# Kernel optimization log

Measured on AMD Instinct MI355X. Metric: run time of the kernel, lower is better.

The kernel has to match this reference:

```python
import jax, jax.numpy as jnp
import numpy as np

EPS = 1e-5
GROUPS = 32


def group_norm(x, gamma, beta):
    b, c, h, w = x.shape
    xg = x.reshape(b, GROUPS, c // GROUPS, h, w)
    mu = xg.mean(axis=(2, 3, 4), keepdims=True)
    var = xg.var(axis=(2, 3, 4), keepdims=True)
    xn = ((xg - mu) * jax.lax.rsqrt(var + EPS)).reshape(b, c, h, w)
    return xn * gamma[None, :, None, None] + beta[None, :, None, None]


def setup_inputs() -> dict:
    key = jax.random.key(0)
    ks = jax.random.split(key, 4)
    b, c, h, w = 4, 512, 64, 64
    x = jax.random.normal(ks[0], (b, c, h, w), dtype=jnp.float32)
    gn_w = jnp.ones((c,), jnp.float32)
    gn_b = jnp.zeros((c,), jnp.float32)
    qkv_w = jax.random.normal(ks[1], (3 * c, c), dtype=jnp.float32) * (c ** -0.5)
    qkv_b = jnp.zeros((3 * c,), jnp.float32)
    out_w = jax.random.normal(ks[2], (c, c), dtype=jnp.float32) * (c ** -0.5)
    out_b = jnp.zeros((c,), jnp.float32)
    return {"x": x, "gn_w": gn_w, "gn_b": gn_b, "qkv_w": qkv_w,
            "qkv_b": qkv_b, "out_w": out_w, "out_b": out_b}


def reference(x, gn_w, gn_b, qkv_w, qkv_b, out_w, out_b):
    b, c, hh, ww = x.shape
    n = hh * ww
    h = group_norm(x, gn_w, gn_b)
    # 1x1 conv == per-pixel matmul over channels
    qkv = jnp.einsum('bchw,oc->bohw', h, qkv_w) + qkv_b[None, :, None, None]
    q, k, v = jnp.split(qkv, 3, axis=1)
    q = q.transpose(0, 2, 3, 1).reshape(b, n, c)   # (b, n, c)
    k = k.reshape(b, c, n)                          # (b, c, n)
    v = v.transpose(0, 2, 3, 1).reshape(b, n, c)   # (b, n, c)
    attn = jax.nn.softmax(jnp.einsum('bnc,bcm->bnm', q, k) * (c ** -0.5), axis=-1)
    out = jnp.einsum('bnm,bmc->bnc', attn, v)
    out = out.reshape(b, hh, ww, c).transpose(0, 3, 1, 2)
    out = jnp.einsum('bchw,oc->bohw', out, out_w) + out_b[None, :, None, None]
    return out + x
```

## Files before the change

### kernel.cpp

```cpp
#include <hip/hip_runtime.h>
#include <cmath>

#define NB 4
#define NC 512
#define NN 4096
#define ATTN_SCALE 0.04419417382415922f

typedef __bf16 bf16x8 __attribute__((ext_vector_type(8)));
typedef float floatx4 __attribute__((ext_vector_type(4)));

__device__ __forceinline__ unsigned short f2bf(float f) {
    union { float f; unsigned int u; } v; v.f = f;
    return (unsigned short)((v.u + 0x7fffu + ((v.u >> 16) & 1u)) >> 16);
}
__device__ __forceinline__ unsigned short f2bf_trunc(float f) {
    union { float f; unsigned int u; } v; v.f = f;
    return (unsigned short)(v.u >> 16);
}

__device__ __forceinline__ void gload_lds16(const unsigned short* gp, unsigned short* lp) {
    __builtin_amdgcn_global_load_lds(
        (const __attribute__((address_space(1))) void*)gp,
        (__attribute__((address_space(3))) void*)lp, 16, 0, 0);
}

template<int N> __device__ __forceinline__ void wait_vmcnt() {
    if constexpr (N == 0) asm volatile("s_waitcnt vmcnt(0)" ::: "memory");
    else if constexpr (N == 2) asm volatile("s_waitcnt vmcnt(2)" ::: "memory");
    else if constexpr (N == 3) asm volatile("s_waitcnt vmcnt(3)" ::: "memory");
    else if constexpr (N == 4) asm volatile("s_waitcnt vmcnt(4)" ::: "memory");
    else if constexpr (N == 6) asm volatile("s_waitcnt vmcnt(6)" ::: "memory");
}

__global__ __launch_bounds__(256) void gn_partial_kernel(
    const float* __restrict__ x, float* __restrict__ part)
{
    int blk = blockIdx.x;
    int bg = blk >> 3, sub = blk & 7;
    const float4* xv = (const float4*)(x + (size_t)bg * 16 * NN + (size_t)sub * 8192);
    float s1 = 0.f, s2 = 0.f;
#pragma unroll
    for (int i = 0; i < 8; ++i) {
        float4 v = xv[threadIdx.x + i * 256];
        s1 += v.x + v.y + v.z + v.w;
        s2 += v.x * v.x + v.y * v.y + v.z * v.z + v.w * v.w;
    }
#pragma unroll
    for (int off = 32; off; off >>= 1) {
        s1 += __shfl_xor(s1, off, 64);
        s2 += __shfl_xor(s2, off, 64);
    }
    __shared__ float r1[4], r2[4];
    int lane = threadIdx.x & 63, w = threadIdx.x >> 6;
    if (lane == 0) { r1[w] = s1; r2[w] = s2; }
    __syncthreads();
    if (threadIdx.x == 0) {
        part[blk * 2]     = r1[0] + r1[1] + r1[2] + r1[3];
        part[blk * 2 + 1] = r2[0] + r2[1] + r2[2] + r2[3];
    }
}

__global__ __launch_bounds__(128) void gn_final_kernel(
    const float* __restrict__ part, const float* __restrict__ gw,
    const float* __restrict__ gb, float* __restrict__ ss)
{
    int tg = threadIdx.x;
    int b = tg >> 5, g = tg & 31;
    float s1 = 0.f, s2 = 0.f;
#pragma unroll
    for (int s = 0; s < 8; ++s) {
        s1 += part[(tg * 8 + s) * 2];
        s2 += part[(tg * 8 + s) * 2 + 1];
    }
    float mean = s1 * (1.0f / 65536.0f);
    float var  = s2 * (1.0f / 65536.0f) - mean * mean;
    float rstd = rsqrtf(var + 1e-5f);
#pragma unroll
    for (int i = 0; i < 16; ++i) {
        int c = g * 16 + i;
        float sc = rstd * gw[c];
        ss[b * NC + c] = sc;
        ss[2048 + b * NC + c] = gb[c] - mean * sc;
    }
}

__global__ __launch_bounds__(256) void wconv_kernel(
    const float* __restrict__ qkv_w, const float* __restrict__ out_w,
    unsigned short* __restrict__ wq, unsigned short* __restrict__ wo)
{
    int i = blockIdx.x * 256 + threadIdx.x;
    const int NQ = 1536 * 512;
    if (i < NQ) wq[i] = f2bf(qkv_w[i]);
    else        wo[i - NQ] = f2bf(out_w[i - NQ]);
}

__global__ __launch_bounds__(256) void htnorm_kernel(
    const float* __restrict__ x, const float* __restrict__ ss,
    unsigned short* __restrict__ ht)
{
    int b = blockIdx.z;
    int c0 = blockIdx.y * 32, n0 = blockIdx.x * 32;
    __shared__ float T[32][33];
    int tx = threadIdx.x & 31, ty = threadIdx.x >> 5;
    const float* xb = x + ((size_t)b * NC + c0) * NN;
    const float* sc = ss + b * NC + c0;
    const float* sh = ss + 2048 + b * NC + c0;
#pragma unroll
    for (int i = 0; i < 4; ++i) {
        int c = ty + i * 8;
        T[c][tx] = xb[(size_t)c * NN + n0 + tx] * sc[c] + sh[c];
    }
    __syncthreads();
    unsigned short* hb = ht + ((size_t)b * NN + n0) * NC + c0;
#pragma unroll
    for (int i = 0; i < 4; ++i) {
        int n = ty + i * 8;
        hb[(size_t)n * NC + tx] = f2bf(T[tx][n]);
    }
}

template<int MODE, int BM, int BN, int KD, int MINB, int PIPE>
__global__ __launch_bounds__(256, MINB) void mfma_gemm(
    const unsigned short* __restrict__ Abase,
    const unsigned short* __restrict__ Bbase,
    const float* __restrict__ e0, const float* __restrict__ e1,
    float* __restrict__ outf,
    unsigned short* __restrict__ ob0, unsigned short* __restrict__ ob1)
{
    constexpr int NT = KD / 32;
    constexpr int FI = BM / 32;
    constexpr int FJ = BN / 32;
    constexpr int LPS = BM / 64 + BN / 64;
    const size_t bnc = (size_t)NN * NC;
    const size_t bss = (size_t)NN * NN;

    int z, m0, n0;
    if constexpr (MODE == 2) {
        const int id = blockIdx.x;
        const int xcd = id & 7, j = id >> 3;
        const int mi = xcd * 8 + (j & 7);
        z = mi >> 4; m0 = (mi & 15) * BM; n0 = (j >> 3) * BN;
    } else {
        z = blockIdx.z; m0 = blockIdx.y * BM; n0 = blockIdx.x * BN;
    }

    const unsigned short* A;
    const unsigned short* B;
    if constexpr (MODE == 0)      { A = Abase + (size_t)z * bnc; B = Bbase; }
    else if constexpr (MODE == 1) { A = Abase; B = Bbase + (size_t)z * bnc; }
    else if constexpr (MODE == 2) { A = Abase + (size_t)z * bnc; B = Bbase + (size_t)z * bnc; }
    else                          { A = Abase; B = Bbase + (size_t)z * bnc; }

    __shared__ __attribute__((aligned(16))) unsigned short As[3][BM * 32];
    __shared__ __attribute__((aligned(16))) unsigned short Bs[3][BN * 32];

    const int t = threadIdx.x;
    const int lane = t & 63;
    const int w = t >> 6;
    const int wr = w >> 1, wc = w & 1;

    const int sr = w * 16 + (lane >> 2);
    const int scs = ((lane & 3) ^ ((lane >> 3) & 3)) * 8;
    const int lds_elem = w * 512;
    const int kslot = lane >> 4;

    floatx4 acc[FI][FJ] = {};

    auto stage = [&](int buf, int tile) {
        const int k0 = tile * 32;
#pragma unroll
        for (int s = 0; s < BM / 64; ++s)
            gload_lds16(A + (size_t)(m0 + s * 64 + sr) * KD + k0 + scs,
                        &As[buf][s * 2048 + lds_elem]);
#pragma unroll
        for (int s = 0; s < BN / 64; ++s)
            gload_lds16(B + (size_t)(n0 + s * 64 + sr) * KD + k0 + scs,
                        &Bs[buf][s * 2048 + lds_elem]);
    };

    auto ds_frags = [&](int buf, bf16x8* af, bf16x8* bfr) {
#pragma unroll
        for (int i = 0; i < FI; ++i) {
            const int ra = wr * (BM / 2) + i * 16 + (lane & 15);
            af[i] = *(const bf16x8*)(&As[buf][ra * 32 + ((kslot ^ ((ra >> 1) & 3)) * 8)]);
        }
#pragma unroll
        for (int j = 0; j < FJ; ++j) {
            const int rb = wc * (BN / 2) + j * 16 + (lane & 15);
            bfr[j] = *(const bf16x8*)(&Bs[buf][rb * 32 + ((kslot ^ ((rb >> 1) & 3)) * 8)]);
        }
    };

    auto mfma_all = [&](const bf16x8* af, const bf16x8* bfr) {
#pragma unroll
        for (int i = 0; i < FI; ++i)
#pragma unroll
            for (int j = 0; j < FJ; ++j)
                acc[i][j] = __builtin_amdgcn_mfma_f32_16x16x32_bf16(
                    af[i], bfr[j], acc[i][j], 0, 0, 0);
    };

    if constexpr (PIPE == 0) {
        bf16x8 af[FI], bfr[FJ];
        stage(0, 0);
        stage(1, 1);
        wait_vmcnt<LPS>();
        __builtin_amdgcn_s_barrier();
#pragma unroll
        for (int kt = 0; kt < NT - 2; ++kt) {
            stage((kt + 2) % 3, kt + 2);
            ds_frags(kt % 3, af, bfr);
            mfma_all(af, bfr);
            asm volatile("s_waitcnt lgkmcnt(0)" ::: "memory");
            wait_vmcnt<LPS>();
            __builtin_amdgcn_s_barrier();
        }
        ds_frags((NT - 2) % 3, af, bfr);
        mfma_all(af, bfr);
        asm volatile("s_waitcnt lgkmcnt(0)" ::: "memory");
        wait_vmcnt<0>();
        __builtin_amdgcn_s_barrier();
        ds_frags((NT - 1) % 3, af, bfr);
        mfma_all(af, bfr);
    } else {
        bf16x8 afA[FI], bfA[FJ], afB[FI], bfB[FJ];
        stage(0, 0);
        stage(1, 1);
        wait_vmcnt<LPS>();
        __builtin_amdgcn_s_barrier();
        ds_frags(0, afA, bfA);
        asm volatile("s_waitcnt lgkmcnt(0)" ::: "memory");
#pragma unroll
        for (int kp = 0; kp < (NT - 2) / 2; ++kp) {
            const int kt = kp * 2;
            stage((kt + 2) % 3, kt + 2);
            wait_vmcnt<LPS>();
            __builtin_amdgcn_s_barrier();
            ds_frags((kt + 1) % 3, afB, bfB);
            mfma_all(afA, bfA);
            asm volatile("s_waitcnt lgkmcnt(0)" ::: "memory");
            stage((kt + 3) % 3, kt + 3);
            wait_vmcnt<LPS>();
            __builtin_amdgcn_s_barrier();
            ds_frags((kt + 2) % 3, afA, bfA);
            mfma_all(afB, bfB);
            asm volatile("s_waitcnt lgkmcnt(0)" ::: "memory");
        }
        wait_vmcnt<0>();
        __builtin_amdgcn_s_barrier();
        ds_frags((NT - 1) % 3, afB, bfB);
        mfma_all(afA, bfA);
        asm volatile("s_waitcnt lgkmcnt(0)" ::: "memory");
        mfma_all(afB, bfB);
    }

    const int fr = lane >> 4;
    const int fc = lane & 15;

    if constexpr (MODE == 2) {
        float rs[FI][4];
#pragma unroll
        for (int i = 0; i < FI; ++i)
#pragma unroll
            for (int r = 0; r < 4; ++r) rs[i][r] = 0.f;
#pragma unroll
        for (int i = 0; i < FI; ++i) {
#pragma unroll
            for (int j = 0; j < FJ; ++j) {
                int n = n0 + wc * (BN / 2) + j * 16 + fc;
                int mbase = m0 + wr * (BM / 2) + i * 16 + fr * 4;
#pragma unroll
                for (int r = 0; r < 4; ++r) {
                    float e = __expf(acc[i][j][r]);
                    ob0[(size_t)z * bss + (size_t)(mbase + r) * NN + n] = f2bf_trunc(e);
                    rs[i][r] += e;
                }
            }
        }
#pragma unroll
        for (int i = 0; i < FI; ++i) {
#pragma unroll
            for (int r = 0; r < 4; ++r) {
                float v = rs[i][r];
                v += __shfl_xor(v, 1, 16);
                v += __shfl_xor(v, 2, 16);
                v += __shfl_xor(v, 4, 16);
                v += __shfl_xor(v, 8, 16);
                if (fc == 0) {
                    int m = m0 + wr * (BM / 2) + i * 16 + fr * 4 + r;
                    atomicAdd(&outf[z * NN + m], v);
                }
            }
        }
        return;
    }

#pragma unroll
    for (int i = 0; i < FI; ++i) {
#pragma unroll
        for (int j = 0; j < FJ; ++j) {
            int n = n0 + wc * (BN / 2) + j * 16 + fc;
            int mbase = m0 + wr * (BM / 2) + i * 16 + fr * 4;
#pragma unroll
            for (int r = 0; r < 4; ++r) {
                int m = mbase + r;
                float val = acc[i][j][r];
                if constexpr (MODE == 0) {
                    val += e0[n];
                    if (n < 512) ob0[((size_t)z * NN + m) * NC + n] = f2bf(val * ATTN_SCALE);
                    else         ob1[((size_t)z * NN + m) * NC + (n - 512)] = f2bf(val);
                } else if constexpr (MODE == 1) {
                    val += e0[1024 + m];
                    ob0[((size_t)z * NC + m) * NN + n] = f2bf(val);
                } else {
                    size_t idx = ((size_t)z * NC + m) * NN + n;
                    outf[idx] = val + e0[m] + e1[idx];
                }
            }
        }
    }
}

__global__ __launch_bounds__(256, 2) void pv_gemm(
    const unsigned short* __restrict__ Abase,
    const unsigned short* __restrict__ Bbase,
    const float* __restrict__ L,
    unsigned short* __restrict__ Ob)
{
    const int id = blockIdx.x;
    const int xcd = id & 7;
    const int j0 = id >> 3;
    const int ct = j0 & 3;
    const int p = (j0 >> 2) * 8 + xcd;
    const int ptile = p & 31, z = p >> 5;

    const size_t bss = (size_t)NN * NN, bnc = (size_t)NN * NC;
    const unsigned short* A = Abase + (size_t)z * bss;
    const unsigned short* B = Bbase + (size_t)z * bnc;
    const int m0 = ptile * 128;
    const int n0 = ct * 128;

    __shared__ __attribute__((aligned(16))) unsigned short As[2][128 * 64];
    __shared__ __attribute__((aligned(16))) unsigned short Bs[2][128 * 64];

    const int t = threadIdx.x;
    const int lane = t & 63;
    const int w = t >> 6;
    const int wr = w >> 1, wc = w & 1;

    const int sr = w * 8 + (lane >> 3);
    const int scs = ((lane & 7) ^ (lane >> 3)) * 8;
    const int lds_elem = w * 512;

    floatx4 acc[4][4] = {};

    auto stage = [&](int buf, int k0) {
#pragma unroll
        for (int s = 0; s < 4; ++s)
            gload_lds16(A + (size_t)(m0 + s * 32 + sr) * NN + k0 + scs,
                        &As[buf][s * 2048 + lds_elem]);
#pragma unroll
        for (int s = 0; s < 4; ++s)
            gload_lds16(B + (size_t)(n0 + s * 32 + sr) * NN + k0 + scs,
                        &Bs[buf][s * 2048 + lds_elem]);
    };

    auto compute = [&](int buf) {
#pragma unroll
        for (int kk = 0; kk < 2; ++kk) {
            bf16x8 af[4], bfr[4];
#pragma unroll
            for (int i = 0; i < 4; ++i) {
                const int ra = wr * 64 + i * 16 + (lane & 15);
                af[i] = *(const bf16x8*)(&As[buf][ra * 64 +
                        (((kk * 4 + (lane >> 4)) ^ (ra & 7)) * 8)]);
            }
#pragma unroll
            for (int jf = 0; jf < 4; ++jf) {
                const int rb = wc * 64 + jf * 16 + (lane & 15);
                bfr[jf] = *(const bf16x8*)(&Bs[buf][rb * 64 +
                        (((kk * 4 + (lane >> 4)) ^ (rb & 7)) * 8)]);
            }
#pragma unroll
            for (int i = 0; i < 4; ++i)
#pragma unroll
                for (int jf = 0; jf < 4; ++jf)
                    acc[i][jf] = __builtin_amdgcn_mfma_f32_16x16x32_bf16(
                        af[i], bfr[jf], acc[i][jf], 0, 0, 0);
        }
    };

    stage(0, 0);
    asm volatile("s_waitcnt vmcnt(0)" ::: "memory");
    __builtin_amdgcn_s_barrier();
    for (int kc = 0; kc < 63; ++kc) {
        stage((kc + 1) & 1, (kc + 1) * 64);
        compute(kc & 1);
        asm volatile("s_waitcnt lgkmcnt(0)" ::: "memory");
        asm volatile("s_waitcnt vmcnt(0)" ::: "memory");
        __builtin_amdgcn_s_barrier();
    }
    compute(1);

    const int fr = lane >> 4;
    const int fc = lane & 15;
#pragma unroll
    for (int i = 0; i < 4; ++i) {
#pragma unroll
        for (int r = 0; r < 4; ++r) {
            int m = m0 + wr * 64 + i * 16 + fr * 4 + r;
            float linv = 1.0f / L[z * NN + m];
#pragma unroll
            for (int jf = 0; jf < 4; ++jf) {
                int n = n0 + wc * 64 + jf * 16 + fc;
                Ob[(size_t)z * bnc + (size_t)m * NC + n] = f2bf(acc[i][jf][r] * linv);
            }
        }
    }
}

extern "C" void kernel_launch(void* const* d_in, const int* in_sizes, int n_in,
                              void* d_out, int out_size, void* d_ws, size_t ws_size,
                              hipStream_t stream)
{
    const float* x     = (const float*)d_in[0];
    const float* gn_w  = (const float*)d_in[1];
    const float* gn_b  = (const float*)d_in[2];
    const float* qkv_w = (const float*)d_in[3];
    const float* qkv_b = (const float*)d_in[4];
    const float* out_w = (const float*)d_in[5];
    const float* out_b = (const float*)d_in[6];
    float* out = (float*)d_out;

    const size_t bnc = (size_t)NN * NC;
    char* w = (char*)d_ws;
    float* ss   = (float*)w;                 w += 16384;
    float* part = (float*)w;                 w += 8192;
    float* Lsum = (float*)w;                 w += (size_t)NB * NN * 4;
    unsigned short* wq = (unsigned short*)w; w += (size_t)1536 * 512 * 2;
    unsigned short* wo = (unsigned short*)w; w += (size_t)512 * 512 * 2;
    unsigned short* qt = (unsigned short*)w; w += NB * bnc * 2;
    unsigned short* kt = (unsigned short*)w; w += NB * bnc * 2;
    unsigned short* vt = (unsigned short*)w; w += NB * bnc * 2;
    unsigned short* SP = (unsigned short*)w; w += (size_t)NB * NN * NN * 2;
    unsigned short* ht = SP;
    unsigned short* Ob = qt;

    hipMemsetAsync(Lsum, 0, (size_t)NB * NN * sizeof(float), stream);

    gn_partial_kernel<<<1024, 256, 0, stream>>>(x, part);
    gn_final_kernel<<<1, 128, 0, stream>>>(part, gn_w, gn_b, ss);
    wconv_kernel<<<(1536 * 512 + 512 * 512) / 256, 256, 0, stream>>>(qkv_w, out_w, wq, wo);
    htnorm_kernel<<<dim3(NN / 32, NC / 32, NB), 256, 0, stream>>>(x, ss, ht);

    mfma_gemm<0, 128, 128, 512, 2, 1><<<dim3(1024 / 128, NN / 128, NB), 256, 0, stream>>>(
        ht, wq, qkv_b, nullptr, nullptr, qt, kt);
    mfma_gemm<1, 64, 128, 512, 4, 1><<<dim3(NN / 128, 512 / 64, NB), 256, 0, stream>>>(
        wq + (size_t)1024 * 512, ht, qkv_b, nullptr, nullptr, vt, nullptr);

    mfma_gemm<2, 256, 128, 512, 2, 0><<<dim3(2048), 256, 0, stream>>>(
        qt, kt, nullptr, nullptr, Lsum, SP, nullptr);
    pv_gemm<<<dim3(512), 256, 0, stream>>>(SP, vt, Lsum, Ob);

    mfma_gemm<4, 64, 128, 512, 4, 1><<<dim3(NN / 128, 512 / 64, NB), 256, 0, stream>>>(
        wo, Ob, out_b, x, out, nullptr, nullptr);
}
```

Baseline: 341.6 us.

## Enlarge PV GEMM tile to 256x128 with 512 threads and triple-buffered loads

The P·V GEMM kernel now uses 512-thread blocks, each computing a 256x128 output tile. The launch grid halves to 256 blocks, and the block-to-tile mapping changes so each XCD pair handles a single batch. The single-stage double buffer becomes a three-deep ring with partial vmcnt waits, so two chunks are in flight while one is computed. The aim is better reuse of the B tile, a lower count of redundant A/B loads, and hidden global-load latency. The cost is more LDS per block (144KB) and one resident block per CU, which reduces occupancy. 256 blocks may also underfill the CUs.

```diff
diff --git a/kernel.cpp b/kernel.cpp
--- a/kernel.cpp
+++ b/kernel.cpp
@@ -321,7 +321,7 @@
     }
 }
 
-__global__ __launch_bounds__(256, 2) void pv_gemm(
+__global__ __launch_bounds__(512, 1) void pv_gemm(
     const unsigned short* __restrict__ Abase,
     const unsigned short* __restrict__ Bbase,
     const float* __restrict__ L,
@@ -329,40 +329,41 @@
 {
     const int id = blockIdx.x;
     const int xcd = id & 7;
-    const int j0 = id >> 3;
-    const int ct = j0 & 3;
-    const int p = (j0 >> 2) * 8 + xcd;
-    const int ptile = p & 31, z = p >> 5;
+    const int j = id >> 3;
+    const int z = xcd >> 1;
+    const int ct = (xcd & 1) * 2 + (j & 1);
+    const int pt = j >> 1;
+    const int m0 = pt * 256;
+    const int n0 = ct * 128;
 
     const size_t bss = (size_t)NN * NN, bnc = (size_t)NN * NC;
     const unsigned short* A = Abase + (size_t)z * bss;
     const unsigned short* B = Bbase + (size_t)z * bnc;
-    const int m0 = ptile * 128;
-    const int n0 = ct * 128;
-
-    __shared__ __attribute__((aligned(16))) unsigned short As[2][128 * 64];
-    __shared__ __attribute__((aligned(16))) unsigned short Bs[2][128 * 64];
+
+    __shared__ __attribute__((aligned(16))) unsigned short As[3][256 * 64];
+    __shared__ __attribute__((aligned(16))) unsigned short Bs[3][128 * 64];
 
     const int t = threadIdx.x;
     const int lane = t & 63;
     const int w = t >> 6;
     const int wr = w >> 1, wc = w & 1;
 
-    const int sr = w * 8 + (lane >> 3);
-    const int scs = ((lane & 7) ^ (lane >> 3)) * 8;
-    const int lds_elem = w * 512;
+    const int sra = t >> 3;
+    const int scs = ((t & 7) ^ (sra & 7)) * 8;
+    const int sdst = t * 8;
 
     floatx4 acc[4][4] = {};
 
-    auto stage = [&](int buf, int k0) {
+    auto stage = [&](int buf, int chunk) {
+        const int k0 = chunk * 64;
 #pragma unroll
         for (int s = 0; s < 4; ++s)
-            gload_lds16(A + (size_t)(m0 + s * 32 + sr) * NN + k0 + scs,
-                        &As[buf][s * 2048 + lds_elem]);
-#pragma unroll
-        for (int s = 0; s < 4; ++s)
-            gload_lds16(B + (size_t)(n0 + s * 32 + sr) * NN + k0 + scs,
-                        &Bs[buf][s * 2048 + lds_elem]);
+            gload_lds16(A + (size_t)(m0 + s * 64 + sra) * NN + k0 + scs,
+                        &As[buf][s * 4096 + sdst]);
+#pragma unroll
+        for (int s = 0; s < 2; ++s)
+            gload_lds16(B + (size_t)(n0 + s * 64 + sra) * NN + k0 + scs,
+                        &Bs[buf][s * 4096 + sdst]);
     };
 
     auto compute = [&](int buf) {
@@ -391,16 +392,22 @@
     };
 
     stage(0, 0);
-    asm volatile("s_waitcnt vmcnt(0)" ::: "memory");
+    stage(1, 1);
+    wait_vmcnt<6>();
     __builtin_amdgcn_s_barrier();
-    for (int kc = 0; kc < 63; ++kc) {
-        stage((kc + 1) & 1, (kc + 1) * 64);
-        compute(kc & 1);
+
+    for (int kc = 0; kc < 62; ++kc) {
+        stage((kc + 2) % 3, kc + 2);
+        compute(kc % 3);
         asm volatile("s_waitcnt lgkmcnt(0)" ::: "memory");
-        asm volatile("s_waitcnt vmcnt(0)" ::: "memory");
+        wait_vmcnt<6>();
         __builtin_amdgcn_s_barrier();
     }
-    compute(1);
+    compute(62 % 3);
+    asm volatile("s_waitcnt lgkmcnt(0)" ::: "memory");
+    wait_vmcnt<0>();
+    __builtin_amdgcn_s_barrier();
+    compute(63 % 3);
 
     const int fr = lane >> 4;
     const int fc = lane & 15;
@@ -460,7 +467,7 @@
 
     mfma_gemm<2, 256, 128, 512, 2, 0><<<dim3(2048), 256, 0, stream>>>(
         qt, kt, nullptr, nullptr, Lsum, SP, nullptr);
-    pv_gemm<<<dim3(512), 256, 0, stream>>>(SP, vt, Lsum, Ob);
+    pv_gemm<<<dim3(256), 512, 0, stream>>>(SP, vt, Lsum, Ob);
 
     mfma_gemm<4, 64, 128, 512, 4, 1><<<dim3(NN / 128, 512 / 64, NB), 256, 0, stream>>>(
         wo, Ob, out_b, x, out, nullptr, nullptr);
```

Result: slower. 360.9 us (+5.7%).
